# Performance work log

Measured on AMD Instinct MI355X. Metric: run time of the kernel, lower is better.

## Reference

```python
import jax, jax.numpy as jnp
import numpy as np

N, IN_DIM, OUT_DIM = 2048, 128, 64
ALPHA = 0.2  # LeakyReLU negative slope


def setup_inputs() -> dict:
    key = jax.random.key(0)
    k1, k2, k3 = jax.random.split(key, 3)
    H = jax.random.normal(k1, (N, IN_DIM), dtype=jnp.float32)
    # Xavier-uniform-like init for W [out_dim, in_dim] (torch Linear weight layout)
    limit_w = float(np.sqrt(6.0 / (IN_DIM + OUT_DIM)))
    W = jax.random.uniform(k2, (OUT_DIM, IN_DIM), dtype=jnp.float32,
                           minval=-limit_w, maxval=limit_w)
    limit_a = float(np.sqrt(6.0 / (OUT_DIM + 1)))
    a = jax.random.uniform(k3, (OUT_DIM,), dtype=jnp.float32,
                           minval=-limit_a, maxval=limit_a)
    return {"H": H, "W": W, "a": a}


def reference(H, W, a):
    # Wh: [N, D]
    Wh = H @ W.T
    # e[i, j] = leakyrelu(Wh[i] + Wh[j]) . a   -> [N, N]
    e = jnp.einsum('ijd,d->ij',
                   jax.nn.leaky_relu(Wh[:, None, :] + Wh[None, :, :],
                                     negative_slope=ALPHA),
                   a)
    attention = jax.nn.softmax(e, axis=1)  # softmax over j (columns)
    return attention @ Wh  # [N, D]
```

## Files before the change

### kernel.cpp

```cpp
#include <hip/hip_runtime.h>
#include <hip/hip_fp16.h>

#define N 2048
#define IN_DIM 128
#define D 64
#define ALPHA 0.2f
#define TI 4
#define BLK 512
#define NW (BLK / 64)


typedef _Float16 half2v __attribute__((ext_vector_type(2)));

__device__ __forceinline__ unsigned short f2h_rne(float f) {
  return __half_as_ushort(__float2half(f));
}

__device__ __forceinline__ float dot2abs(unsigned s2, unsigned w2,
                                         unsigned a2, float acc) {
  half2v sv = __builtin_bit_cast(half2v, s2);
  half2v wv = __builtin_bit_cast(half2v, w2);
  half2v t = sv + wv;
  unsigned tu = __builtin_bit_cast(unsigned, t) & 0x7fff7fffu;
  return __builtin_amdgcn_fdot2(__builtin_bit_cast(half2v, tu),
                                __builtin_bit_cast(half2v, a2),
                                acc, false);
}

__device__ __forceinline__ float dot2u(unsigned p2, unsigned w2, float acc) {
  return __builtin_amdgcn_fdot2(__builtin_bit_cast(half2v, p2),
                                __builtin_bit_cast(half2v, w2),
                                acc, false);
}

__device__ __forceinline__ unsigned cvt_pk_u(float lo, float hi) {
  return __builtin_bit_cast(unsigned, __builtin_amdgcn_cvt_pkrtz(lo, hi));
}

__global__ __launch_bounds__(512) void wh_kernel(
    const float* __restrict__ H, const float* __restrict__ W,
    const float* __restrict__ a, unsigned short* __restrict__ Whh,
    unsigned int* __restrict__ WhP, unsigned int* __restrict__ WhQ,
    float* __restrict__ bs2, unsigned int* __restrict__ ap2) {
  __shared__ float wlds[D][IN_DIM + 1];
  __shared__ float hl[4 * IN_DIM];
  __shared__ float partial[512];
  __shared__ __align__(16) unsigned short hh[4][D];
  const int t = threadIdx.x;
  const int i0 = blockIdx.x * 4;
  const float L2E = 1.4426950408889634f;

  if (blockIdx.x == 0 && t < D / 2) {
    ap2[t] = (unsigned)f2h_rne(0.4f * a[2 * t]) |
             ((unsigned)f2h_rne(0.4f * a[2 * t + 1]) << 16);
  }

  #pragma unroll
  for (int rep = 0; rep < 4; ++rep) {
    int idx = (rep * 512 + t) * 4;
    float4 w4 = *(const float4*)&W[idx];
    int d = idx >> 7, k = idx & 127;
    wlds[d][k] = w4.x; wlds[d][k + 1] = w4.y;
    wlds[d][k + 2] = w4.z; wlds[d][k + 3] = w4.w;
  }
  if (t < 128)
    *(float4*)&hl[t * 4] = *(const float4*)&H[i0 * IN_DIM + t * 4];
  __syncthreads();

  {
    const int oi = t & 255, kh = t >> 8;
    const int r = oi >> 6, d = oi & 63;
    float acc = 0.f;
    #pragma unroll 8
    for (int k = 0; k < 64; ++k)
      acc = fmaf(hl[r * IN_DIM + kh * 64 + k], wlds[d][kh * 64 + k], acc);
    partial[t] = acc;
  }
  __syncthreads();

  if (t < 256) {
    const int r = t >> 6, d = t & 63;
    const float acc = partial[t] + partial[t + 256];
    const unsigned myh = f2h_rne(acc);
    hh[r][d] = (unsigned short)myh;
    Whh[(i0 + r) * D + d] = (unsigned short)myh;
    const unsigned hq = (unsigned)__shfl_xor((int)myh, 1);
    if (!(d & 1)) WhP[(d >> 1) * N + (i0 + r)] = myh | (hq << 16);
    float pb = a[d] * acc;
    #pragma unroll
    for (int off = 32; off; off >>= 1) pb += __shfl_xor(pb, off);
    if (d == 0) bs2[i0 + r] = fmaf(0.6f * pb, L2E, -6.f);
  }
  __syncthreads();
  if (t < 128) {
    const int pr = t >> 6, d = t & 63;
    const unsigned lo = hh[pr * 2][d], hi = hh[pr * 2 + 1][d];
    WhQ[((i0 >> 1) + pr) * D + d] = lo | (hi << 16);
  }
}

__global__ __launch_bounds__(BLK, 4) void attn_kernel(
    const unsigned short* __restrict__ Whh,
    const unsigned int* __restrict__ WhP,
    const unsigned int* __restrict__ WhQ,
    const float* __restrict__ bs2, const unsigned int* __restrict__ ap2,
    float* __restrict__ out) {
  __shared__ unsigned short p_lds[TI][N];
  __shared__ float red2s[TI][NW];
  __shared__ float part[NW][TI][D];
  __shared__ uint4 stage[TI * 8 + D / 8];

  const int t = threadIdx.x;
  const int i0 = blockIdx.x * TI;
  const int wid = t >> 6, lane = t & 63;

  if (t < TI * 8 + D / 8) {
    stage[t] = (t < TI * 8) ? ((const uint4*)(Whh + i0 * D))[t]
                            : ((const uint4*)ap2)[t - TI * 8];
  }
  __syncthreads();

  const int j0 = t * 4;
  float4 bj = *(const float4*)&bs2[j0];
  float4 ac[TI];
  #pragma unroll
  for (int ti = 0; ti < TI; ++ti) { ac[ti].x = ac[ti].y = ac[ti].z = ac[ti].w = 0.f; }

  const unsigned int* wp = WhP + j0;

  uint4 wbuf[2][4], sbuf[2][TI], abuf[2];
  #pragma unroll
  for (int q = 0; q < 4; ++q) wbuf[0][q] = *(const uint4*)&wp[q * N];
  #pragma unroll
  for (int ti = 0; ti < TI; ++ti) sbuf[0][ti] = stage[ti * 8];
  abuf[0] = stage[TI * 8];

  #pragma unroll
  for (int c = 0; c < D / 8; ++c) {
    const int cur = c & 1, nxt = cur ^ 1;
    if (c < D / 8 - 1) {
      #pragma unroll
      for (int q = 0; q < 4; ++q)
        wbuf[nxt][q] = *(const uint4*)&wp[((c + 1) * 4 + q) * N];
      #pragma unroll
      for (int ti = 0; ti < TI; ++ti) sbuf[nxt][ti] = stage[ti * 8 + c + 1];
      abuf[nxt] = stage[TI * 8 + c + 1];
    }
    #pragma unroll
    for (int q = 0; q < 4; ++q) {
      const unsigned a2 = (q == 0) ? abuf[cur].x : (q == 1) ? abuf[cur].y
                        : (q == 2) ? abuf[cur].z : abuf[cur].w;
      const uint4 w4 = wbuf[cur][q];
      #pragma unroll
      for (int ti = 0; ti < TI; ++ti) {
        const unsigned s2 = (q == 0) ? sbuf[cur][ti].x : (q == 1) ? sbuf[cur][ti].y
                          : (q == 2) ? sbuf[cur][ti].z : sbuf[cur][ti].w;
        ac[ti].x = dot2abs(s2, w4.x, a2, ac[ti].x);
        ac[ti].y = dot2abs(s2, w4.y, a2, ac[ti].y);
        ac[ti].z = dot2abs(s2, w4.z, a2, ac[ti].z);
        ac[ti].w = dot2abs(s2, w4.w, a2, ac[ti].w);
      }
    }
  }

  const int jbase = wid * (N / NW);
  const int hi4 = (lane >> 4) * 4;
  const int col = (lane & 15) * 4;
  uint4 wq[2][2];
  {
    const int r0 = jbase + hi4;
    wq[0][0] = *(const uint4*)&WhQ[(r0 >> 1) * D + col];
    wq[0][1] = *(const uint4*)&WhQ[((r0 >> 1) + 1) * D + col];
  }

  const float L2E = 1.4426950408889634f;
  float s_t[TI];
  #pragma unroll
  for (int ti = 0; ti < TI; ++ti) {
    float4 p4;
    p4.x = __builtin_amdgcn_exp2f(fmaf(ac[ti].x, L2E, bj.x));
    p4.y = __builtin_amdgcn_exp2f(fmaf(ac[ti].y, L2E, bj.y));
    p4.z = __builtin_amdgcn_exp2f(fmaf(ac[ti].z, L2E, bj.z));
    p4.w = __builtin_amdgcn_exp2f(fmaf(ac[ti].w, L2E, bj.w));
    uint2 ph;
    ph.x = cvt_pk_u(p4.x, p4.y);
    ph.y = cvt_pk_u(p4.z, p4.w);
    *(uint2*)&p_lds[ti][j0] = ph;
    s_t[ti] = (p4.x + p4.y) + (p4.z + p4.w);
  }
  #pragma unroll
  for (int off = 32; off; off >>= 1) {
    #pragma unroll
    for (int ti = 0; ti < TI; ++ti)
      s_t[ti] += __shfl_xor(s_t[ti], off);
  }
  if (lane == 0) {
    #pragma unroll
    for (int ti = 0; ti < TI; ++ti) red2s[ti][wid] = s_t[ti];
  }
  __syncthreads();

  float4 acc[TI];
  #pragma unroll
  for (int ti = 0; ti < TI; ++ti) { acc[ti].x = acc[ti].y = acc[ti].z = acc[ti].w = 0.f; }

  uint2 pt[2][TI];
  {
    const int r0 = jbase + hi4;
    #pragma unroll
    for (int ti = 0; ti < TI; ++ti)
      pt[0][ti] = *(const uint2*)&p_lds[ti][r0];
  }

  #pragma unroll
  for (int it = 0; it < (N / NW) / 16; ++it) {
    const int cur = it & 1, nxt = cur ^ 1;
    if (it < (N / NW) / 16 - 1) {
      const int r1 = jbase + (it + 1) * 16 + hi4;
      wq[nxt][0] = *(const uint4*)&WhQ[(r1 >> 1) * D + col];
      wq[nxt][1] = *(const uint4*)&WhQ[((r1 >> 1) + 1) * D + col];
      #pragma unroll
      for (int ti = 0; ti < TI; ++ti)
        pt[nxt][ti] = *(const uint2*)&p_lds[ti][r1];
    }
    #pragma unroll
    for (int ti = 0; ti < TI; ++ti) {
      const unsigned ppA = pt[cur][ti].x;
      const unsigned ppB = pt[cur][ti].y;
      acc[ti].x = dot2u(ppB, wq[cur][1].x, dot2u(ppA, wq[cur][0].x, acc[ti].x));
      acc[ti].y = dot2u(ppB, wq[cur][1].y, dot2u(ppA, wq[cur][0].y, acc[ti].y));
      acc[ti].z = dot2u(ppB, wq[cur][1].z, dot2u(ppA, wq[cur][0].z, acc[ti].z));
      acc[ti].w = dot2u(ppB, wq[cur][1].w, dot2u(ppA, wq[cur][0].w, acc[ti].w));
    }
  }
  #pragma unroll
  for (int ti = 0; ti < TI; ++ti) {
    acc[ti].x += __shfl_xor(acc[ti].x, 16);
    acc[ti].y += __shfl_xor(acc[ti].y, 16);
    acc[ti].z += __shfl_xor(acc[ti].z, 16);
    acc[ti].w += __shfl_xor(acc[ti].w, 16);
    acc[ti].x += __shfl_xor(acc[ti].x, 32);
    acc[ti].y += __shfl_xor(acc[ti].y, 32);
    acc[ti].z += __shfl_xor(acc[ti].z, 32);
    acc[ti].w += __shfl_xor(acc[ti].w, 32);
  }
  if (lane < 16) {
    #pragma unroll
    for (int ti = 0; ti < TI; ++ti)
      *(float4*)&part[wid][ti][lane * 4] = acc[ti];
  }
  __syncthreads();
  if (t < TI * D) {
    const int ti = t >> 6, dd = t & 63;
    float s = 0.f;
    #pragma unroll
    for (int w = 0; w < NW; ++w) s += part[w][ti][dd];
    float4 r0 = *(const float4*)&red2s[ti][0];
    float4 r1 = *(const float4*)&red2s[ti][4];
    float rsum = ((r0.x + r0.y) + (r0.z + r0.w)) +
                 ((r1.x + r1.y) + (r1.z + r1.w));
    out[(i0 + ti) * D + dd] = s * (1.f / rsum);
  }
}

extern "C" void kernel_launch(void* const* d_in, const int* in_sizes, int n_in,
                              void* d_out, int out_size, void* d_ws, size_t ws_size,
                              hipStream_t stream) {
  const float* H = (const float*)d_in[0];
  const float* W = (const float*)d_in[1];
  const float* a = (const float*)d_in[2];
  float* out = (float*)d_out;

  unsigned short* Whh = (unsigned short*)d_ws;
  unsigned int* WhP = (unsigned int*)(Whh + N * D);
  unsigned int* WhQ = WhP + (D / 2) * N;
  float* bs2 = (float*)(WhQ + (N / 2) * D);
  unsigned int* ap2 = (unsigned int*)(bs2 + N);

  wh_kernel<<<N / 4, 512, 0, stream>>>(H, W, a, Whh, WhP, WhQ, bs2, ap2);
  attn_kernel<<<N / TI, BLK, 0, stream>>>(Whh, WhP, WhQ, bs2, ap2, out);
}
```

Baseline: 29.68 us.

## Halve block size and compute eight columns per thread in score phase

Cuts the block from 512 to 256 threads. Each thread now computes scores for 8 columns j instead of 4, so each LDS-staged row and attention value is reused across twice as many columns. The software double-buffering of WhP loads is dropped in favour of plain per-chunk loads, which leaves the compiler to schedule latency hiding. Register pressure rises and there are half as many waves per block, while the final reduction loses its thread guard and sums four wave partials instead of eight.

```diff
diff --git a/kernel.cpp b/kernel.cpp
--- a/kernel.cpp
+++ b/kernel.cpp
@@ -6,8 +6,9 @@
 #define D 64
 #define ALPHA 0.2f
 #define TI 4
-#define BLK 512
+#define BLK 256
 #define NW (BLK / 64)
+#define JPT (N / BLK)
 
 
 typedef _Float16 half2v __attribute__((ext_vector_type(2)));
@@ -120,45 +121,46 @@
   }
   __syncthreads();
 
-  const int j0 = t * 4;
-  float4 bj = *(const float4*)&bs2[j0];
-  float4 ac[TI];
-  #pragma unroll
-  for (int ti = 0; ti < TI; ++ti) { ac[ti].x = ac[ti].y = ac[ti].z = ac[ti].w = 0.f; }
+  const int j0 = t * JPT;
+  float4 bj0 = *(const float4*)&bs2[j0];
+  float4 bj1 = *(const float4*)&bs2[j0 + 4];
+  float ac[TI][JPT];
+  #pragma unroll
+  for (int ti = 0; ti < TI; ++ti)
+    #pragma unroll
+    for (int jj = 0; jj < JPT; ++jj) ac[ti][jj] = 0.f;
 
   const unsigned int* wp = WhP + j0;
 
-  uint4 wbuf[2][4], sbuf[2][TI], abuf[2];
-  #pragma unroll
-  for (int q = 0; q < 4; ++q) wbuf[0][q] = *(const uint4*)&wp[q * N];
-  #pragma unroll
-  for (int ti = 0; ti < TI; ++ti) sbuf[0][ti] = stage[ti * 8];
-  abuf[0] = stage[TI * 8];
-
   #pragma unroll
   for (int c = 0; c < D / 8; ++c) {
-    const int cur = c & 1, nxt = cur ^ 1;
-    if (c < D / 8 - 1) {
-      #pragma unroll
-      for (int q = 0; q < 4; ++q)
-        wbuf[nxt][q] = *(const uint4*)&wp[((c + 1) * 4 + q) * N];
-      #pragma unroll
-      for (int ti = 0; ti < TI; ++ti) sbuf[nxt][ti] = stage[ti * 8 + c + 1];
-      abuf[nxt] = stage[TI * 8 + c + 1];
-    }
+    uint4 wA[4], wB[4];
     #pragma unroll
     for (int q = 0; q < 4; ++q) {
-      const unsigned a2 = (q == 0) ? abuf[cur].x : (q == 1) ? abuf[cur].y
-                        : (q == 2) ? abuf[cur].z : abuf[cur].w;
-      const uint4 w4 = wbuf[cur][q];
+      wA[q] = *(const uint4*)&wp[(c * 4 + q) * N];
+      wB[q] = *(const uint4*)&wp[(c * 4 + q) * N + 4];
+    }
+    const uint4 a4 = stage[TI * 8 + c];
+    uint4 s4[TI];
+    #pragma unroll
+    for (int ti = 0; ti < TI; ++ti) s4[ti] = stage[ti * 8 + c];
+    #pragma unroll
+    for (int q = 0; q < 4; ++q) {
+      const unsigned a2 = (q == 0) ? a4.x : (q == 1) ? a4.y
+                        : (q == 2) ? a4.z : a4.w;
+      const uint4 vA = wA[q], vB = wB[q];
       #pragma unroll
       for (int ti = 0; ti < TI; ++ti) {
-        const unsigned s2 = (q == 0) ? sbuf[cur][ti].x : (q == 1) ? sbuf[cur][ti].y
-                          : (q == 2) ? sbuf[cur][ti].z : sbuf[cur][ti].w;
-        ac[ti].x = dot2abs(s2, w4.x, a2, ac[ti].x);
-        ac[ti].y = dot2abs(s2, w4.y, a2, ac[ti].y);
-        ac[ti].z = dot2abs(s2, w4.z, a2, ac[ti].z);
-        ac[ti].w = dot2abs(s2, w4.w, a2, ac[ti].w);
+        const unsigned s2 = (q == 0) ? s4[ti].x : (q == 1) ? s4[ti].y
+                          : (q == 2) ? s4[ti].z : s4[ti].w;
+        ac[ti][0] = dot2abs(s2, vA.x, a2, ac[ti][0]);
+        ac[ti][1] = dot2abs(s2, vA.y, a2, ac[ti][1]);
+        ac[ti][2] = dot2abs(s2, vA.z, a2, ac[ti][2]);
+        ac[ti][3] = dot2abs(s2, vA.w, a2, ac[ti][3]);
+        ac[ti][4] = dot2abs(s2, vB.x, a2, ac[ti][4]);
+        ac[ti][5] = dot2abs(s2, vB.y, a2, ac[ti][5]);
+        ac[ti][6] = dot2abs(s2, vB.z, a2, ac[ti][6]);
+        ac[ti][7] = dot2abs(s2, vB.w, a2, ac[ti][7]);
       }
     }
   }
@@ -177,16 +179,21 @@
   float s_t[TI];
   #pragma unroll
   for (int ti = 0; ti < TI; ++ti) {
-    float4 p4;
-    p4.x = __builtin_amdgcn_exp2f(fmaf(ac[ti].x, L2E, bj.x));
-    p4.y = __builtin_amdgcn_exp2f(fmaf(ac[ti].y, L2E, bj.y));
-    p4.z = __builtin_amdgcn_exp2f(fmaf(ac[ti].z, L2E, bj.z));
-    p4.w = __builtin_amdgcn_exp2f(fmaf(ac[ti].w, L2E, bj.w));
-    uint2 ph;
-    ph.x = cvt_pk_u(p4.x, p4.y);
-    ph.y = cvt_pk_u(p4.z, p4.w);
-    *(uint2*)&p_lds[ti][j0] = ph;
-    s_t[ti] = (p4.x + p4.y) + (p4.z + p4.w);
+    float p0 = __builtin_amdgcn_exp2f(fmaf(ac[ti][0], L2E, bj0.x));
+    float p1 = __builtin_amdgcn_exp2f(fmaf(ac[ti][1], L2E, bj0.y));
+    float p2 = __builtin_amdgcn_exp2f(fmaf(ac[ti][2], L2E, bj0.z));
+    float p3 = __builtin_amdgcn_exp2f(fmaf(ac[ti][3], L2E, bj0.w));
+    float p4 = __builtin_amdgcn_exp2f(fmaf(ac[ti][4], L2E, bj1.x));
+    float p5 = __builtin_amdgcn_exp2f(fmaf(ac[ti][5], L2E, bj1.y));
+    float p6 = __builtin_amdgcn_exp2f(fmaf(ac[ti][6], L2E, bj1.z));
+    float p7 = __builtin_amdgcn_exp2f(fmaf(ac[ti][7], L2E, bj1.w));
+    uint4 ph;
+    ph.x = cvt_pk_u(p0, p1);
+    ph.y = cvt_pk_u(p2, p3);
+    ph.z = cvt_pk_u(p4, p5);
+    ph.w = cvt_pk_u(p6, p7);
+    *(uint4*)&p_lds[ti][j0] = ph;
+    s_t[ti] = ((p0 + p1) + (p2 + p3)) + ((p4 + p5) + (p6 + p7));
   }
   #pragma unroll
   for (int off = 32; off; off >>= 1) {
@@ -250,15 +257,13 @@
       *(float4*)&part[wid][ti][lane * 4] = acc[ti];
   }
   __syncthreads();
-  if (t < TI * D) {
+  {
     const int ti = t >> 6, dd = t & 63;
     float s = 0.f;
     #pragma unroll
     for (int w = 0; w < NW; ++w) s += part[w][ti][dd];
     float4 r0 = *(const float4*)&red2s[ti][0];
-    float4 r1 = *(const float4*)&red2s[ti][4];
-    float rsum = ((r0.x + r0.y) + (r0.z + r0.w)) +
-                 ((r1.x + r1.y) + (r1.z + r1.w));
+    float rsum = (r0.x + r0.y) + (r0.z + r0.w);
     out[(i0 + ti) * D + dd] = s * (1.f / rsum);
   }
 }
```

Measured after the change: 30.34 us. +2.2%, slower.

## Compute attention-weighted aggregation with MFMA 16x16x32 f16 instead of fdot2

Applied to the files above, without the earlier changes.

Replaces the per-lane fdot2 loop that computes P@Wh, along with its cross-lane shuffle reduction, with MFMA 16x16x32 f16 matrix instructions. Each wave runs 8 k-steps over 4 output-column tiles. The A operand is read from the P rows in LDS with only 4 of the 16 A rows meaningful (TI=4), so 3/4 of each MFMA is wasted. B operands are now fetched as scalar 32-bit global loads with no double buffering, which adds load latency in exchange for removing the fdot2 arithmetic and the shuffles.

```diff
diff --git a/kernel.cpp b/kernel.cpp
--- a/kernel.cpp
+++ b/kernel.cpp
@@ -11,6 +11,8 @@
 
 
 typedef _Float16 half2v __attribute__((ext_vector_type(2)));
+typedef _Float16 half8 __attribute__((ext_vector_type(8)));
+typedef float f32x4 __attribute__((ext_vector_type(4)));
 
 __device__ __forceinline__ unsigned short f2h_rne(float f) {
   return __half_as_ushort(__float2half(f));
@@ -24,12 +26,6 @@
   unsigned tu = __builtin_bit_cast(unsigned, t) & 0x7fff7fffu;
   return __builtin_amdgcn_fdot2(__builtin_bit_cast(half2v, tu),
                                 __builtin_bit_cast(half2v, a2),
-                                acc, false);
-}
-
-__device__ __forceinline__ float dot2u(unsigned p2, unsigned w2, float acc) {
-  return __builtin_amdgcn_fdot2(__builtin_bit_cast(half2v, p2),
-                                __builtin_bit_cast(half2v, w2),
                                 acc, false);
 }
 
@@ -163,14 +159,17 @@
     }
   }
 
-  const int jbase = wid * (N / NW);
-  const int hi4 = (lane >> 4) * 4;
-  const int col = (lane & 15) * 4;
-  uint4 wq[2][2];
-  {
-    const int r0 = jbase + hi4;
-    wq[0][0] = *(const uint4*)&WhQ[(r0 >> 1) * D + col];
-    wq[0][1] = *(const uint4*)&WhQ[((r0 >> 1) + 1) * D + col];
+  const int kbase = wid * (N / NW);
+  const int arow = lane & 3;
+  const int koff = (lane >> 4) * 8;
+  const int bcol = lane & 15;
+  const int brow0 = (lane >> 4) * 4;
+  uint4 bq0[4];
+  #pragma unroll
+  for (int dt = 0; dt < 4; ++dt) {
+    const int base = ((kbase >> 1) + brow0) * D + dt * 16 + bcol;
+    bq0[dt].x = WhQ[base];         bq0[dt].y = WhQ[base + D];
+    bq0[dt].z = WhQ[base + 2 * D]; bq0[dt].w = WhQ[base + 3 * D];
   }
 
   const float L2E = 1.4426950408889634f;
@@ -200,54 +199,37 @@
   }
   __syncthreads();
 
-  float4 acc[TI];
-  #pragma unroll
-  for (int ti = 0; ti < TI; ++ti) { acc[ti].x = acc[ti].y = acc[ti].z = acc[ti].w = 0.f; }
-
-  uint2 pt[2][TI];
-  {
-    const int r0 = jbase + hi4;
-    #pragma unroll
-    for (int ti = 0; ti < TI; ++ti)
-      pt[0][ti] = *(const uint2*)&p_lds[ti][r0];
-  }
-
-  #pragma unroll
-  for (int it = 0; it < (N / NW) / 16; ++it) {
-    const int cur = it & 1, nxt = cur ^ 1;
-    if (it < (N / NW) / 16 - 1) {
-      const int r1 = jbase + (it + 1) * 16 + hi4;
-      wq[nxt][0] = *(const uint4*)&WhQ[(r1 >> 1) * D + col];
-      wq[nxt][1] = *(const uint4*)&WhQ[((r1 >> 1) + 1) * D + col];
-      #pragma unroll
-      for (int ti = 0; ti < TI; ++ti)
-        pt[nxt][ti] = *(const uint2*)&p_lds[ti][r1];
-    }
-    #pragma unroll
-    for (int ti = 0; ti < TI; ++ti) {
-      const unsigned ppA = pt[cur][ti].x;
-      const unsigned ppB = pt[cur][ti].y;
-      acc[ti].x = dot2u(ppB, wq[cur][1].x, dot2u(ppA, wq[cur][0].x, acc[ti].x));
-      acc[ti].y = dot2u(ppB, wq[cur][1].y, dot2u(ppA, wq[cur][0].y, acc[ti].y));
-      acc[ti].z = dot2u(ppB, wq[cur][1].z, dot2u(ppA, wq[cur][0].z, acc[ti].z));
-      acc[ti].w = dot2u(ppB, wq[cur][1].w, dot2u(ppA, wq[cur][0].w, acc[ti].w));
-    }
-  }
-  #pragma unroll
-  for (int ti = 0; ti < TI; ++ti) {
-    acc[ti].x += __shfl_xor(acc[ti].x, 16);
-    acc[ti].y += __shfl_xor(acc[ti].y, 16);
-    acc[ti].z += __shfl_xor(acc[ti].z, 16);
-    acc[ti].w += __shfl_xor(acc[ti].w, 16);
-    acc[ti].x += __shfl_xor(acc[ti].x, 32);
-    acc[ti].y += __shfl_xor(acc[ti].y, 32);
-    acc[ti].z += __shfl_xor(acc[ti].z, 32);
-    acc[ti].w += __shfl_xor(acc[ti].w, 32);
-  }
+  f32x4 acc[4];
+  #pragma unroll
+  for (int dt = 0; dt < 4; ++dt) acc[dt] = (f32x4){0.f, 0.f, 0.f, 0.f};
+
+  #pragma unroll
+  for (int ks = 0; ks < 8; ++ks) {
+    const int jlo = kbase + ks * 32;
+    const uint4 av = *(const uint4*)&p_lds[arow][jlo + koff];
+    const half8 a8 = __builtin_bit_cast(half8, av);
+    #pragma unroll
+    for (int dt = 0; dt < 4; ++dt) {
+      uint4 bv;
+      if (ks == 0) {
+        bv = bq0[dt];
+      } else {
+        const int base = ((jlo >> 1) + brow0) * D + dt * 16 + bcol;
+        bv.x = WhQ[base];         bv.y = WhQ[base + D];
+        bv.z = WhQ[base + 2 * D]; bv.w = WhQ[base + 3 * D];
+      }
+      acc[dt] = __builtin_amdgcn_mfma_f32_16x16x32_f16(
+          a8, __builtin_bit_cast(half8, bv), acc[dt], 0, 0, 0);
+    }
+  }
+
   if (lane < 16) {
     #pragma unroll
-    for (int ti = 0; ti < TI; ++ti)
-      *(float4*)&part[wid][ti][lane * 4] = acc[ti];
+    for (int dt = 0; dt < 4; ++dt) {
+      #pragma unroll
+      for (int r = 0; r < 4; ++r)
+        part[wid][r][dt * 16 + lane] = acc[dt][r];
+    }
   }
   __syncthreads();
   if (t < TI * D) {
```

Measured after the change: 28.64 us. -3.5%, faster.
